# Performance work log

Measured on AMD Instinct MI355X. Metric: run time of the kernel, lower is better.

The kernel has to match this reference:

```python
import jax, jax.numpy as jnp
import numpy as np

D_IN = 1024
D_OUT = 1024
SEQ = 4096


def setup_inputs() -> dict:
    key = jax.random.key(0)
    kx, kq, kk, kv = jax.random.split(key, 4)
    x = jax.random.normal(kx, (SEQ, D_IN), dtype=jnp.float32)
    # torch Linear weights: [d_out, d_in], y = x @ W.T; no bias (qkv_bias=False)
    s = 1.0 / np.sqrt(D_IN)
    Wq = jax.random.uniform(kq, (D_OUT, D_IN), dtype=jnp.float32, minval=-s, maxval=s)
    Wk = jax.random.uniform(kk, (D_OUT, D_IN), dtype=jnp.float32, minval=-s, maxval=s)
    Wv = jax.random.uniform(kv, (D_OUT, D_IN), dtype=jnp.float32, minval=-s, maxval=s)
    return {"x": x, "Wq": Wq, "Wk": Wk, "Wv": Wv}


def reference(x, Wq, Wk, Wv):
    seq = x.shape[0]
    q = x @ Wq.T  # [S, d_out]
    k = x @ Wk.T
    v = x @ Wv.T
    scores = q @ k.T  # [S, S]
    # causal mask: positions j > i masked to -inf (triu, diagonal=1)
    causal = jnp.tril(jnp.ones((seq, seq), dtype=bool))
    scores = jnp.where(causal, scores, -jnp.inf)
    attn = jax.nn.softmax(scores / jnp.sqrt(jnp.float32(q.shape[-1])), axis=-1)
    return attn @ v  # [S, d_out]
```

## Files before the change

### kernel.cpp

```cpp
#include <hip/hip_runtime.h>
#include <hip/hip_bf16.h>
#include <cstdint>
#include <cstddef>


#define SEQQ 4096
#define DDIM 1024

typedef __bf16 bf16x8 __attribute__((ext_vector_type(8)));
typedef float f32x4 __attribute__((ext_vector_type(4)));

__device__ __forceinline__ unsigned short f2bf(float f) {
  unsigned int u = __builtin_bit_cast(unsigned int, f);
  unsigned int r = u + 0x7FFFu + ((u >> 16) & 1u);
  return (unsigned short)(r >> 16);
}

__device__ __forceinline__ void gload_lds16(const void* g, void* lds) {
  __builtin_amdgcn_global_load_lds(
      (__attribute__((address_space(1))) void*)(uintptr_t)g,
      (__attribute__((address_space(3))) void*)(uintptr_t)lds, 16, 0, 0);
}

__global__ __launch_bounds__(256) void cvt_all(const float* __restrict__ x,
                                               const float* __restrict__ Wq,
                                               const float* __restrict__ Wk,
                                               const float* __restrict__ Wv,
                                               unsigned short* __restrict__ xb,
                                               unsigned short* __restrict__ Wcat) {
  int b = blockIdx.x;
  const float* src;
  unsigned short* dst;
  float scale = 1.0f;
  if (b < 4096) {
    src = x; dst = xb;
  } else if (b < 5120) {
    src = Wq; dst = Wcat; scale = 0.03125f; b -= 4096;
  } else if (b < 6144) {
    src = Wk; dst = Wcat + (1u << 20); b -= 5120;
  } else {
    src = Wv; dst = Wcat + (2u << 20); b -= 6144;
  }
  const int i = (b * 256 + threadIdx.x) * 4;
  const float4 v = *reinterpret_cast<const float4*>(src + i);
  ushort4 o;
  o.x = f2bf(v.x * scale);
  o.y = f2bf(v.y * scale);
  o.z = f2bf(v.z * scale);
  o.w = f2bf(v.w * scale);
  *reinterpret_cast<ushort4*>(dst + i) = o;
}

#define GEMM_PRE()                                                          \
  __shared__ unsigned short As[2][16384] __attribute__((aligned(16)));      \
  __shared__ unsigned short Bs[2][16384] __attribute__((aligned(16)));      \
  const int tid = threadIdx.x;                                              \
  const int wave = tid >> 6, lane = tid & 63;                               \
  const int wr = (wave >> 2) * 128, wc = (wave & 3) * 64;                   \
  f32x4 acc[8][4] = {};                                                     \
  int offA[8], offB[4];                                                     \
  {                                                                         \
    const int cb = (lane >> 4) * 16;                                        \
    const int rA = wr + (lane & 15);                                        \
    _Pragma("unroll")                                                       \
    for (int m = 0; m < 8; ++m) {                                           \
      int o = (rA + m * 16) * 64 + cb;                                      \
      offA[m] = o ^ (((o >> 9) & 1) << 5);                                  \
    }                                                                       \
    const int rB = wc + (lane & 15);                                        \
    _Pragma("unroll")                                                       \
    for (int n = 0; n < 4; ++n) {                                           \
      int o = (rB + n * 16) * 64 + cb;                                      \
      offB[n] = o ^ (((o >> 9) & 1) << 5);                                  \
    }                                                                       \
  }

#define BAR asm volatile("s_barrier" ::: "memory")

#define RD_A(SLOT, MH)                                                     \
  _Pragma("unroll")                                                        \
  for (int mm = 0; mm < 4; ++mm)                                           \
    _Pragma("unroll")                                                      \
    for (int kk = 0; kk < 2; ++kk)                                         \
      aF[mm][kk] = *(const bf16x8*)(ldsA + (SLOT) * 32768 + kk * 16384 +   \
                                    offA[(MH) * 4 + mm]);

#define RD_B(SLOT, NP, BS)                                                 \
  _Pragma("unroll")                                                        \
  for (int nn = 0; nn < 2; ++nn)                                           \
    _Pragma("unroll")                                                      \
    for (int kk = 0; kk < 2; ++kk)                                         \
      BS[nn][kk] = *(const bf16x8*)(ldsB + (SLOT) * 32768 + kk * 16384 +   \
                                    offB[(NP) * 2 + nn]);

#define MFMA16(MH, NP, BS)                                                 \
  __builtin_amdgcn_s_setprio(1);                                           \
  _Pragma("unroll")                                                        \
  for (int kk = 0; kk < 2; ++kk)                                           \
    _Pragma("unroll")                                                      \
    for (int mm = 0; mm < 4; ++mm)                                         \
      _Pragma("unroll")                                                    \
      for (int nn = 0; nn < 2; ++nn)                                       \
        acc[(MH) * 4 + mm][(NP) * 2 + nn] =                                \
            __builtin_amdgcn_mfma_f32_16x16x32_bf16(                       \
                aF[mm][kk], BS[nn][kk],                                    \
                acc[(MH) * 4 + mm][(NP) * 2 + nn], 0, 0, 0);               \
  __builtin_amdgcn_s_setprio(0);

#define STGQ(SLOT, KOFS, Q)                                                \
  {                                                                        \
    const int lofs = (SLOT) * 32768 + ((Q) & 1) * 16384 + wave * 1024;     \
    const int sofs = (KOFS) + ((Q) & 1) * 64;                              \
    if ((Q) < 2) {                                                         \
      gload_lds16(bA0 + sofs, ldsA + lofs);                                \
      gload_lds16(bA1 + sofs, ldsA + lofs + 8192);                         \
    } else {                                                               \
      gload_lds16(bB0 + sofs, ldsB + lofs);                                \
      gload_lds16(bB1 + sofs, ldsB + lofs + 8192);                         \
    }                                                                      \
  }

#define GEMM_LOOP(ABASE, LDA, BBASE, LDB, S0, S1)                          \
  do {                                                                     \
    const int ni = ((S1) - (S0)) >> 1;                                     \
    const size_t lda2 = (size_t)(LDA) * 2, ldb2 = (size_t)(LDB) * 2;       \
    const int srow = wave * 16 + (lane >> 2);                              \
    const int scb = ((lane & 3) * 16) ^ (((lane >> 5) & 1) << 5);          \
    const char* bA0 = (const char*)(ABASE) + (size_t)srow * lda2 +         \
                      (size_t)(S0) * 128 + scb;                            \
    const char* bA1 = bA0 + 128 * lda2;                                    \
    const char* bB0 = (const char*)(BBASE) + (size_t)srow * ldb2 +         \
                      (size_t)(S0) * 128 + scb;                            \
    const char* bB1 = bB0 + 128 * ldb2;                                    \
    char* ldsA = (char*)&As[0][0];                                         \
    char* ldsB = (char*)&Bs[0][0];                                         \
    bf16x8 aF[4][2], b0[2][2], b1[2][2];                                   \
                                     \
    STGQ(0, 0, 0); STGQ(0, 0, 1); STGQ(0, 0, 2); STGQ(0, 0, 3);            \
    STGQ(1, 128, 0);                                                       \
    asm volatile("s_waitcnt vmcnt(2)" ::: "memory");                       \
    BAR;                                                                   \
    for (int i = 0; i < ni; ++i) {                                         \
      const int k0 = i * 256;                                              \
      const bool st = (i + 1 < ni);                                        \
                                                                  \
      RD_A(0, 0); RD_B(0, 0, b0);                                          \
      STGQ(1, k0 + 128, 1);                                                \
      BAR; MFMA16(0, 0, b0); BAR;                                          \
                                                                  \
      RD_B(0, 1, b1);                                                      \
      STGQ(1, k0 + 128, 2);                                                \
      BAR; MFMA16(0, 1, b1); BAR;                                          \
                                                                  \
      RD_A(0, 1);                                                          \
      STGQ(1, k0 + 128, 3);                                                \
      BAR; MFMA16(1, 0, b0); BAR;                                          \
                                                                  \
      if (st) {                                                            \
        STGQ(0, k0 + 256, 0);                                              \
        asm volatile("s_waitcnt vmcnt(2)" ::: "memory");                   \
      } else {                                                             \
        asm volatile("s_waitcnt vmcnt(0)" ::: "memory");                   \
      }                                                                    \
      BAR; MFMA16(1, 1, b1); BAR;                                          \
                                                                  \
      RD_A(1, 0); RD_B(1, 0, b0);                                          \
      if (st) STGQ(0, k0 + 256, 1);                                        \
      BAR; MFMA16(0, 0, b0); BAR;                                          \
                                                                  \
      RD_B(1, 1, b1);                                                      \
      if (st) STGQ(0, k0 + 256, 2);                                        \
      BAR; MFMA16(0, 1, b1); BAR;                                          \
                                                                  \
      RD_A(1, 1);                                                          \
      if (st) STGQ(0, k0 + 256, 3);                                        \
      BAR; MFMA16(1, 0, b0); BAR;                                          \
                                                                  \
      if (st) {                                                            \
        STGQ(1, k0 + 384, 0);                                              \
        asm volatile("s_waitcnt vmcnt(2)" ::: "memory");                   \
        BAR;                                                               \
        MFMA16(1, 1, b1);                                                  \
        BAR;                                                               \
      } else {                                                             \
        MFMA16(1, 1, b1);                                                  \
      }                                                                    \
    }                                                                      \
  } while (0)

__global__ __launch_bounds__(512, 1) void gemm_qkv(const unsigned short* __restrict__ X,
                                                   const unsigned short* __restrict__ W,
                                                   unsigned short* __restrict__ Qb,
                                                   unsigned short* __restrict__ Kb,
                                                   unsigned short* __restrict__ Vt) {
  GEMM_PRE();
  const int brow = blockIdx.y * 256, bcol = blockIdx.x * 256;
  GEMM_LOOP(X + (size_t)brow * DDIM, DDIM, W + (size_t)bcol * DDIM, DDIM, 0, 16);
  const int region = bcol >> 10;
  const int lcol = bcol & 1023;
  const int c0 = wc + (lane & 15);
  const int r0 = wr + ((lane >> 4) << 2);
  if (region < 2) {
    unsigned short* dst = (region == 0) ? Qb : Kb;
#pragma unroll
    for (int m = 0; m < 8; ++m) {
      const int r = brow + r0 + m * 16;
#pragma unroll
      for (int n = 0; n < 4; ++n) {
        const int c = lcol + c0 + n * 16;
#pragma unroll
        for (int j = 0; j < 4; ++j)
          dst[(size_t)(r + j) * DDIM + c] = f2bf(acc[m][n][j]);
      }
    }
  } else {
#pragma unroll
    for (int m = 0; m < 8; ++m) {
      const int r = brow + r0 + m * 16;
#pragma unroll
      for (int n = 0; n < 4; ++n) {
        const int c = lcol + c0 + n * 16;
        ushort4 pk;
        pk.x = f2bf(acc[m][n][0]);
        pk.y = f2bf(acc[m][n][1]);
        pk.z = f2bf(acc[m][n][2]);
        pk.w = f2bf(acc[m][n][3]);
        *reinterpret_cast<ushort4*>(Vt + (size_t)c * SEQQ + r) = pk;
      }
    }
  }
}

__global__ __launch_bounds__(512, 1) void gemm_qkt(const unsigned short* __restrict__ Qb,
                                                   const unsigned short* __restrict__ Kb,
                                                   unsigned short* __restrict__ S) {
  const int bi = blockIdx.y, bj = blockIdx.x;
  if (bj > bi) return;
  GEMM_PRE();
  const int brow = bi * 256, bcol = bj * 256;
  GEMM_LOOP(Qb + (size_t)brow * DDIM, DDIM, Kb + (size_t)bcol * DDIM, DDIM, 0, 16);
  const int c0 = wc + (lane & 15);
  const int r0 = wr + ((lane >> 4) << 2);
#pragma unroll
  for (int m = 0; m < 8; ++m) {
    const int r = brow + r0 + m * 16;
#pragma unroll
    for (int n = 0; n < 4; ++n) {
      const int c = bcol + c0 + n * 16;
#pragma unroll
      for (int j = 0; j < 4; ++j) {
        unsigned short o = (c > r + j) ? (unsigned short)0xFF80
                                       : f2bf(acc[m][n][j]);
        S[(size_t)(r + j) * SEQQ + c] = o;
      }
    }
  }
}

__global__ __launch_bounds__(256) void softmax_causal(unsigned short* __restrict__ S) {
  const int row = blockIdx.x;
  const int L = ((row >> 8) + 1) << 8;
  unsigned short* Srow = S + (size_t)row * SEQQ;
  __shared__ float red[4];
  const int tid = threadIdx.x;
  const int lane = tid & 63, wave = tid >> 6;

  float x[16];
  bool have[2];
  float m = -3.0e38f;
#pragma unroll
  for (int it = 0; it < 2; ++it) {
    const int j = tid * 8 + it * 2048;
    have[it] = (j < L);
    if (have[it]) {
      const uint4 v = *reinterpret_cast<const uint4*>(Srow + j);
      const unsigned u[4] = {v.x, v.y, v.z, v.w};
#pragma unroll
      for (int q = 0; q < 4; ++q) {
        x[it * 8 + q * 2] = __builtin_bit_cast(float, u[q] << 16);
        x[it * 8 + q * 2 + 1] = __builtin_bit_cast(float, u[q] & 0xFFFF0000u);
      }
#pragma unroll
      for (int q = 0; q < 8; ++q) m = fmaxf(m, x[it * 8 + q]);
    }
  }
#pragma unroll
  for (int o = 32; o; o >>= 1) m = fmaxf(m, __shfl_xor(m, o));
  if (lane == 0) red[wave] = m;
  __syncthreads();
  m = fmaxf(fmaxf(red[0], red[1]), fmaxf(red[2], red[3]));
  __syncthreads();

  float sum = 0.f;
#pragma unroll
  for (int it = 0; it < 2; ++it)
    if (have[it]) {
#pragma unroll
      for (int q = 0; q < 8; ++q) {
        x[it * 8 + q] = __expf(x[it * 8 + q] - m);
        sum += x[it * 8 + q];
      }
    }
#pragma unroll
  for (int o = 32; o; o >>= 1) sum += __shfl_xor(sum, o);
  if (lane == 0) red[wave] = sum;
  __syncthreads();
  sum = red[0] + red[1] + red[2] + red[3];
  const float inv = 1.0f / sum;

#pragma unroll
  for (int it = 0; it < 2; ++it)
    if (have[it]) {
      const int j = tid * 8 + it * 2048;
      unsigned u[4];
#pragma unroll
      for (int q = 0; q < 4; ++q) {
        u[q] = (unsigned)f2bf(x[it * 8 + q * 2] * inv) |
               ((unsigned)f2bf(x[it * 8 + q * 2 + 1] * inv) << 16);
      }
      *reinterpret_cast<uint4*>(Srow + j) = make_uint4(u[0], u[1], u[2], u[3]);
    }
}

__device__ __forceinline__ int pv_nc(int bi) { return (bi >> 2) + 1; }
__device__ __forceinline__ int pv_rcbase(int bi) {
  const int g = bi >> 2, r = bi & 3;
  return 2 * g * (g - 1) + r * g;
}

__global__ __launch_bounds__(512, 1) void gemm_pv_split(const unsigned short* __restrict__ P,
                                                        const unsigned short* __restrict__ Vt,
                                                        float* __restrict__ O,
                                                        float* __restrict__ part) {
  const int bj = blockIdx.x, bi = blockIdx.y, ck = blockIdx.z;
  const int nc = pv_nc(bi);
  if (ck >= nc) return;
  const int kt = (bi + 1) * 4;
  const int W = 2 * ((kt + 2 * nc - 1) / (2 * nc));
  const int s0 = ck * W;
  const int s1 = min(s0 + W, kt);
  if (s0 >= s1) return;

  GEMM_PRE();
  const int brow = bi * 256, bcol = bj * 256;
  GEMM_LOOP(P + (size_t)brow * SEQQ, SEQQ, Vt + (size_t)bcol * SEQQ, SEQQ, s0, s1);
  const int c0 = wc + (lane & 15);
  const int r0 = wr + ((lane >> 4) << 2);
  if (ck == 0) {
#pragma unroll
    for (int m = 0; m < 8; ++m) {
      const int r = brow + r0 + m * 16;
#pragma unroll
      for (int n = 0; n < 4; ++n) {
        const int c = bcol + c0 + n * 16;
#pragma unroll
        for (int j = 0; j < 4; ++j)
          O[(size_t)(r + j) * DDIM + c] = acc[m][n][j];
      }
    }
  } else {
    float* tile = part + ((size_t)(pv_rcbase(bi) + (ck - 1)) * 4 + bj) * 65536;
#pragma unroll
    for (int m = 0; m < 8; ++m) {
      const int lr = r0 + m * 16;
#pragma unroll
      for (int n = 0; n < 4; ++n) {
        const int lc = c0 + n * 16;
#pragma unroll
        for (int j = 0; j < 4; ++j)
          tile[(lr + j) * 256 + lc] = acc[m][n][j];
      }
    }
  }
}

__global__ __launch_bounds__(256) void reduce_pv(float* __restrict__ O,
                                                 const float* __restrict__ part) {
  const int idx = blockIdx.x * 256 + threadIdx.x;
  const int r = 1024 + (idx >> 8);
  const int cc = (idx & 255) * 4;
  const int bi = r >> 8;
  const int nparts = bi >> 2;
  const int rcb = pv_rcbase(bi);
  const int bj = cc >> 8;
  const int lr = r & 255, lc = cc & 255;
  float4 acc = *reinterpret_cast<float4*>(O + (size_t)r * DDIM + cc);
  for (int k = 0; k < nparts; ++k) {
    const float4 p = *reinterpret_cast<const float4*>(
        part + ((size_t)(rcb + k) * 4 + bj) * 65536 + lr * 256 + lc);
    acc.x += p.x; acc.y += p.y; acc.z += p.z; acc.w += p.w;
  }
  *reinterpret_cast<float4*>(O + (size_t)r * DDIM + cc) = acc;
}

extern "C" void kernel_launch(void* const* d_in, const int* in_sizes, int n_in,
                              void* d_out, int out_size, void* d_ws, size_t ws_size,
                              hipStream_t stream) {
  (void)in_sizes; (void)n_in; (void)out_size; (void)ws_size;
  const float* x = (const float*)d_in[0];
  const float* Wq = (const float*)d_in[1];
  const float* Wk = (const float*)d_in[2];
  const float* Wv = (const float*)d_in[3];
  float* out = (float*)d_out;

  char* ws = (char*)d_ws;
  unsigned short* xb   = (unsigned short*)(ws);
  unsigned short* Wcat = (unsigned short*)(ws + ((size_t)8 << 20));
  unsigned short* Qb   = (unsigned short*)(ws + ((size_t)14 << 20));
  unsigned short* Kb   = (unsigned short*)(ws + ((size_t)22 << 20));
  unsigned short* Vt   = (unsigned short*)(ws + ((size_t)30 << 20));
  unsigned short* S    = (unsigned short*)(ws + ((size_t)38 << 20));
  float* part = (float*)ws;

  cvt_all<<<7168, 256, 0, stream>>>(x, Wq, Wk, Wv, xb, Wcat);
  gemm_qkv<<<dim3(12, 16), 512, 0, stream>>>(xb, Wcat, Qb, Kb, Vt);
  gemm_qkt<<<dim3(16, 16), 512, 0, stream>>>(Qb, Kb, S);
  softmax_causal<<<SEQQ, 256, 0, stream>>>(S);
  gemm_pv_split<<<dim3(4, 16, 4), 512, 0, stream>>>(S, Vt, out, part);
  reduce_pv<<<3072, 256, 0, stream>>>(out, part);
}
```

Baseline: 128.5 us.

## Restructure GEMM mainloop to per-k-half phases with full B-fragment reuse

Rewrites the double-buffered GEMM main loop so each phase covers one 32-wide k-slice and reads all four B fragments plus four A fragments, issuing 16 MFMAs per phase instead of splitting the work across N halves. The loop now handles one 128-wide k tile per iteration with the slot alternating, rather than unrolling two tiles. It adds explicit lgkmcnt(0) waits and changes the prefetch order and vmcnt thresholds. The intent is fewer LDS reads per MFMA and a simpler schedule, at the cost of different register pressure and altered load/compute overlap.

```diff
diff --git a/kernel.cpp b/kernel.cpp
--- a/kernel.cpp
+++ b/kernel.cpp
@@ -76,35 +76,28 @@
   }
 
 #define BAR asm volatile("s_barrier" ::: "memory")
-
-#define RD_A(SLOT, MH)                                                     \
+#define LGKM0 asm volatile("s_waitcnt lgkmcnt(0)" ::: "memory")
+
+#define RD_A4(SLOT, MH, KK)                                                \
+  _Pragma("unroll")                                                        \
+  for (int mm = 0; mm < 4; ++mm)                                           \
+    aF[mm] = *(const bf16x8*)(ldsA + (SLOT) * 32768 + (KK) * 16384 +       \
+                              offA[(MH) * 4 + mm]);
+
+#define RD_B4(SLOT, KK)                                                    \
+  _Pragma("unroll")                                                        \
+  for (int nn = 0; nn < 4; ++nn)                                           \
+    bF[nn] = *(const bf16x8*)(ldsB + (SLOT) * 32768 + (KK) * 16384 +       \
+                              offB[nn]);
+
+#define MFMA16Q(MH)                                                        \
+  __builtin_amdgcn_s_setprio(1);                                           \
   _Pragma("unroll")                                                        \
   for (int mm = 0; mm < 4; ++mm)                                           \
     _Pragma("unroll")                                                      \
-    for (int kk = 0; kk < 2; ++kk)                                         \
-      aF[mm][kk] = *(const bf16x8*)(ldsA + (SLOT) * 32768 + kk * 16384 +   \
-                                    offA[(MH) * 4 + mm]);
-
-#define RD_B(SLOT, NP, BS)                                                 \
-  _Pragma("unroll")                                                        \
-  for (int nn = 0; nn < 2; ++nn)                                           \
-    _Pragma("unroll")                                                      \
-    for (int kk = 0; kk < 2; ++kk)                                         \
-      BS[nn][kk] = *(const bf16x8*)(ldsB + (SLOT) * 32768 + kk * 16384 +   \
-                                    offB[(NP) * 2 + nn]);
-
-#define MFMA16(MH, NP, BS)                                                 \
-  __builtin_amdgcn_s_setprio(1);                                           \
-  _Pragma("unroll")                                                        \
-  for (int kk = 0; kk < 2; ++kk)                                           \
-    _Pragma("unroll")                                                      \
-    for (int mm = 0; mm < 4; ++mm)                                         \
-      _Pragma("unroll")                                                    \
-      for (int nn = 0; nn < 2; ++nn)                                       \
-        acc[(MH) * 4 + mm][(NP) * 2 + nn] =                                \
-            __builtin_amdgcn_mfma_f32_16x16x32_bf16(                       \
-                aF[mm][kk], BS[nn][kk],                                    \
-                acc[(MH) * 4 + mm][(NP) * 2 + nn], 0, 0, 0);               \
+    for (int nn = 0; nn < 4; ++nn)                                         \
+      acc[(MH) * 4 + mm][nn] = __builtin_amdgcn_mfma_f32_16x16x32_bf16(    \
+          aF[mm], bF[nn], acc[(MH) * 4 + mm][nn], 0, 0, 0);                \
   __builtin_amdgcn_s_setprio(0);
 
 #define STGQ(SLOT, KOFS, Q)                                                \
@@ -122,7 +115,7 @@
 
 #define GEMM_LOOP(ABASE, LDA, BBASE, LDB, S0, S1)                          \
   do {                                                                     \
-    const int ni = ((S1) - (S0)) >> 1;                                     \
+    const int nt = (S1) - (S0);                                            \
     const size_t lda2 = (size_t)(LDA) * 2, ldb2 = (size_t)(LDB) * 2;       \
     const int srow = wave * 16 + (lane >> 2);                              \
     const int scb = ((lane & 3) * 16) ^ (((lane >> 5) & 1) << 5);          \
@@ -134,57 +127,47 @@
     const char* bB1 = bB0 + 128 * ldb2;                                    \
     char* ldsA = (char*)&As[0][0];                                         \
     char* ldsB = (char*)&Bs[0][0];                                         \
-    bf16x8 aF[4][2], b0[2][2], b1[2][2];                                   \
-                                     \
-    STGQ(0, 0, 0); STGQ(0, 0, 1); STGQ(0, 0, 2); STGQ(0, 0, 3);            \
-    STGQ(1, 128, 0);                                                       \
-    asm volatile("s_waitcnt vmcnt(2)" ::: "memory");                       \
+    bf16x8 aF[4], bF[4];                                                   \
+                                         \
+    STGQ(0, 0, 0); STGQ(0, 0, 2); STGQ(0, 0, 1); STGQ(0, 0, 3);            \
+    asm volatile("s_waitcnt vmcnt(0)" ::: "memory");                       \
     BAR;                                                                   \
-    for (int i = 0; i < ni; ++i) {                                         \
-      const int k0 = i * 256;                                              \
-      const bool st = (i + 1 < ni);                                        \
-                                                                  \
-      RD_A(0, 0); RD_B(0, 0, b0);                                          \
-      STGQ(1, k0 + 128, 1);                                                \
-      BAR; MFMA16(0, 0, b0); BAR;                                          \
-                                                                  \
-      RD_B(0, 1, b1);                                                      \
-      STGQ(1, k0 + 128, 2);                                                \
-      BAR; MFMA16(0, 1, b1); BAR;                                          \
-                                                                  \
-      RD_A(0, 1);                                                          \
-      STGQ(1, k0 + 128, 3);                                                \
-      BAR; MFMA16(1, 0, b0); BAR;                                          \
-                                                                  \
+    for (int t = 0; t < nt; ++t) {                                         \
+      const int S = t & 1;                                                 \
+      const int kof = (t + 1) * 128;                                       \
+      const bool st = (t + 1 < nt);                                        \
+                                                       \
+      RD_A4(S, 0, 0); RD_B4(S, 0);                                         \
+      if (st) STGQ(S ^ 1, kof, 0);                                         \
+      BAR; LGKM0;                                                          \
+      MFMA16Q(0);                                                          \
+      BAR;                                                                 \
+                                                       \
+      RD_A4(S, 1, 0);                                                      \
       if (st) {                                                            \
-        STGQ(0, k0 + 256, 0);                                              \
-        asm volatile("s_waitcnt vmcnt(2)" ::: "memory");                   \
+        STGQ(S ^ 1, kof, 2);                                               \
+        asm volatile("s_waitcnt vmcnt(4)" ::: "memory");                   \
       } else {                                                             \
         asm volatile("s_waitcnt vmcnt(0)" ::: "memory");                   \
       }                                                                    \
-      BAR; MFMA16(1, 1, b1); BAR;                                          \
-                                                                  \
-      RD_A(1, 0); RD_B(1, 0, b0);                                          \
-      if (st) STGQ(0, k0 + 256, 1);                                        \
-      BAR; MFMA16(0, 0, b0); BAR;                                          \
-                                                                  \
-      RD_B(1, 1, b1);                                                      \
-      if (st) STGQ(0, k0 + 256, 2);                                        \
-      BAR; MFMA16(0, 1, b1); BAR;                                          \
-                                                                  \
-      RD_A(1, 1);                                                          \
-      if (st) STGQ(0, k0 + 256, 3);                                        \
-      BAR; MFMA16(1, 0, b0); BAR;                                          \
-                                                                  \
+      BAR; LGKM0;                                                          \
+      MFMA16Q(1);                                                          \
+      BAR;                                                                 \
+                                                       \
+      RD_A4(S, 0, 1); RD_B4(S, 1);                                         \
+      if (st) STGQ(S ^ 1, kof, 1);                                         \
+      BAR; LGKM0;                                                          \
+      MFMA16Q(0);                                                          \
+      BAR;                                                                 \
+                                                       \
+      RD_A4(S, 1, 1);                                                      \
       if (st) {                                                            \
-        STGQ(1, k0 + 384, 0);                                              \
-        asm volatile("s_waitcnt vmcnt(2)" ::: "memory");                   \
-        BAR;                                                               \
-        MFMA16(1, 1, b1);                                                  \
-        BAR;                                                               \
-      } else {                                                             \
-        MFMA16(1, 1, b1);                                                  \
+        STGQ(S ^ 1, kof, 3);                                               \
+        asm volatile("s_waitcnt vmcnt(4)" ::: "memory");                   \
       }                                                                    \
+      BAR; LGKM0;                                                          \
+      MFMA16Q(1);                                                          \
+      if (st) BAR;                                                         \
     }                                                                      \
   } while (0)
 
```

Result: slower. 132.7 us (+3.2%).
